# Kernel optimization log

Hardware: AMD Instinct MI355X
Metric: run time of the kernel (lower is better)

## Reference

```python
import jax, jax.numpy as jnp
import numpy as np

B, L, C, H, K = 2, 2048, 1024, 16, 32
Dh = C // H


def setup_inputs() -> dict:
    key = jax.random.key(0)
    ks = jax.random.split(key, 6)
    x = jax.random.normal(ks[0], (B, L, C), dtype=jnp.float32)
    # indices: self index first, then K-1 random neighbors (shared across batch & heads)
    self_idx = jnp.arange(L, dtype=jnp.int32).reshape(1, L, 1)
    rand_idx = jax.random.randint(ks[1], (1, L, K - 1), 0, L, dtype=jnp.int32)
    idx = jnp.concatenate([self_idx, rand_idx], axis=-1)  # (1, L, K)
    s = 1.0 / np.sqrt(C)
    Wq = jax.random.normal(ks[2], (C, C), dtype=jnp.float32) * s
    Wk = jax.random.normal(ks[3], (C, C), dtype=jnp.float32) * s
    Wv = jax.random.normal(ks[4], (C, C), dtype=jnp.float32) * s
    Wo = jax.random.normal(ks[5], (C, C), dtype=jnp.float32) * s
    return {"x": x, "idx": idx, "Wq": Wq, "Wk": Wk, "Wv": Wv, "Wo": Wo}


def reference(x, idx, Wq, Wk, Wv, Wo):
    # projections (torch Linear: y = x @ W.T), reshape to (B, H, L, Dh)
    def heads(y):
        return y.reshape(B, L, H, Dh).transpose(0, 2, 1, 3)

    q = heads(x @ Wq.T)
    k = heads(x @ Wk.T)
    v = heads(x @ Wv.T)

    idx0 = idx[0]  # (L, K) shared across batch and heads
    k_n = jnp.take(k, idx0, axis=2)  # (B, H, L, K, Dh)
    v_n = jnp.take(v, idx0, axis=2)  # (B, H, L, K, Dh)

    q = q / jnp.sqrt(jnp.asarray(Dh, q.dtype))
    attn = jnp.einsum("bhld,bhlkd->bhlk", q, k_n)
    attn = jax.nn.softmax(attn, axis=-1)
    out = jnp.einsum("bhlk,bhlkd->bhld", attn, v_n)
    out = out.transpose(0, 2, 1, 3).reshape(B, L, C)
    return out @ Wo.T
```

## Files before the change

### kernel.cpp

```cpp
#include <hip/hip_runtime.h>
#include <hip/hip_bf16.h>

#define B_  2
#define L_  2048
#define C_  1024
#define H_  16
#define K_  32
#define DH_ 64
#define M_  (B_ * L_)

typedef __hip_bfloat16 bf16;
typedef __attribute__((ext_vector_type(4))) float f32x4;
typedef __attribute__((ext_vector_type(8))) short short8;
typedef __attribute__((ext_vector_type(8))) unsigned short u16x8;

__device__ inline unsigned short f2bf(float f) {
    __hip_bfloat16 h = __float2bfloat16(f);
    return *reinterpret_cast<unsigned short*>(&h);
}
__device__ inline float bf2f(unsigned short u) {
    return __uint_as_float(((unsigned)u) << 16);
}
__device__ inline void gld_lds16(const bf16* g, bf16* l) {
    __builtin_amdgcn_global_load_lds(
        (const __attribute__((address_space(1))) void*)g,
        (__attribute__((address_space(3))) void*)l,
        16, 0, 0);
}

__global__ void __launch_bounds__(256) cvt_all(
    const float* __restrict__ x,  const float* __restrict__ wq,
    const float* __restrict__ wk, const float* __restrict__ wv,
    const float* __restrict__ wo,
    bf16* __restrict__ xb,  bf16* __restrict__ wqb, bf16* __restrict__ wkb,
    bf16* __restrict__ wvb, bf16* __restrict__ wob)
{
    int g = blockIdx.x * 256 + threadIdx.x;
    const float* src; bf16* dst; int o;
    if (g < 1048576)      { src = x;  dst = xb;  o = g; }
    else if (g < 1310720) { src = wq; dst = wqb; o = g - 1048576; }
    else if (g < 1572864) { src = wk; dst = wkb; o = g - 1310720; }
    else if (g < 1835008) { src = wv; dst = wvb; o = g - 1572864; }
    else                  { src = wo; dst = wob; o = g - 1835008; }
    float4 f = reinterpret_cast<const float4*>(src)[o];
    ushort4 u;
    u.x = f2bf(f.x); u.y = f2bf(f.y); u.z = f2bf(f.z); u.w = f2bf(f.w);
    reinterpret_cast<ushort4*>(dst)[o] = u;
}

struct GemmArgs {
    const bf16* A;
    const bf16* W[3];
    bf16* Yb[3];
    float* Yf;
    float scale0;
};

template<int OUT_F32>
__global__ void __launch_bounds__(256) gemm_nt(GemmArgs ga)
{
    __shared__ bf16 As[128 * 64];
    __shared__ bf16 Bs[128 * 64];

    const int m0  = blockIdx.x * 128;
    const int nt  = blockIdx.y;
    const int seg = nt >> 3;
    const int n0  = (nt & 7) * 128;
    const bf16* __restrict__ A = ga.A;
    const bf16* __restrict__ W = ga.W[seg];
    const float scale = (seg == 0) ? ga.scale0 : 1.0f;

    const int t    = threadIdx.x;
    const int lane = t & 63;
    const int w    = t >> 6;
    const int wm   = w >> 1;
    const int wn   = w & 1;

    const int subrow = lane >> 3;
    const int kc     = lane & 7;

    f32x4 acc[4][4] = {};

    for (int kt = 0; kt < 16; ++kt) {
        const int k0 = kt * 64;
        if (kt) __syncthreads();
        #pragma unroll
        for (int i = 0; i < 4; ++i) {
            const int r0  = w * 32 + i * 8;
            const int row = r0 + subrow;
            const int kcs = kc ^ (subrow & 7);
            gld_lds16(A + (size_t)(m0 + row) * 1024 + k0 + kcs * 8, As + r0 * 64);
        }
        #pragma unroll
        for (int i = 0; i < 4; ++i) {
            const int r0  = w * 32 + i * 8;
            const int row = r0 + subrow;
            const int kcs = kc ^ (subrow & 7);
            gld_lds16(W + (size_t)(n0 + row) * 1024 + k0 + kcs * 8, Bs + r0 * 64);
        }
        __syncthreads();
        #pragma unroll
        for (int ks = 0; ks < 2; ++ks) {
            short8 af[4], bfv[4];
            #pragma unroll
            for (int mf = 0; mf < 4; ++mf) {
                const int row    = wm * 64 + mf * 16 + (lane & 15);
                const int kchunk = ks * 4 + (lane >> 4);
                const int pc     = kchunk ^ (row & 7);
                af[mf] = *reinterpret_cast<const short8*>(As + row * 64 + pc * 8);
            }
            #pragma unroll
            for (int nf = 0; nf < 4; ++nf) {
                const int row    = wn * 64 + nf * 16 + (lane & 15);
                const int kchunk = ks * 4 + (lane >> 4);
                const int pc     = kchunk ^ (row & 7);
                bfv[nf] = *reinterpret_cast<const short8*>(Bs + row * 64 + pc * 8);
            }
            #pragma unroll
            for (int mf = 0; mf < 4; ++mf)
                #pragma unroll
                for (int nf = 0; nf < 4; ++nf)
                    acc[mf][nf] = __builtin_amdgcn_mfma_f32_16x16x32_bf16(
                        af[mf], bfv[nf], acc[mf][nf], 0, 0, 0);
        }
    }

    #pragma unroll
    for (int mf = 0; mf < 4; ++mf) {
        #pragma unroll
        for (int nf = 0; nf < 4; ++nf) {
            const int row = m0 + wm * 64 + mf * 16 + ((lane >> 4) << 2);
            const int col = n0 + wn * 64 + nf * 16 + (lane & 15);
            #pragma unroll
            for (int r = 0; r < 4; ++r) {
                const float val = acc[mf][nf][r] * scale;
                if constexpr (OUT_F32) {
                    ga.Yf[(size_t)(row + r) * 1024 + col] = val;
                } else {
                    ga.Yb[seg][(size_t)(row + r) * 1024 + col] = __float2bfloat16(val);
                }
            }
        }
    }
}

__global__ void __launch_bounds__(64) attn_knn(
    const bf16* __restrict__ qg, const bf16* __restrict__ kg,
    const bf16* __restrict__ vg, const int* __restrict__ idx,
    bf16* __restrict__ ao)
{
    const int wb = blockIdx.x;
    const int l  = blockIdx.y;
    const int b  = wb >> 2;
    const int wg = wb & 3;

    const int lane = threadIdx.x;
    const int hw   = lane >> 4;
    const int h    = wg * 4 + hw;
    const int sl   = lane & 15;
    const int half = sl >> 3;
    const int c8   = sl & 7;

    const size_t rowq = (size_t)b * L_ + l;
    const unsigned short* kg16 = reinterpret_cast<const unsigned short*>(kg);
    const unsigned short* vg16 = reinterpret_cast<const unsigned short*>(vg);

    int4 iv[4];
    #pragma unroll
    for (int i = 0; i < 4; ++i)
        iv[i] = reinterpret_cast<const int4*>(idx + l * K_ + half * 16)[i];

    u16x8 qv = *reinterpret_cast<const u16x8*>(
        reinterpret_cast<const unsigned short*>(qg) + rowq * C_ + h * DH_ + c8 * 8);
    float qf[8];
    #pragma unroll
    for (int e = 0; e < 8; ++e) qf[e] = bf2f(qv[e]);

    float s[16];
    #pragma unroll
    for (int jj = 0; jj < 16; ++jj) {
        const int4 q4 = iv[jj >> 2];
        const int row = (jj & 3) == 0 ? q4.x : (jj & 3) == 1 ? q4.y
                       : (jj & 3) == 2 ? q4.z : q4.w;
        const u16x8 kv = *reinterpret_cast<const u16x8*>(
            kg16 + ((size_t)b * L_ + row) * C_ + h * DH_ + c8 * 8);
        float acc = 0.f;
        #pragma unroll
        for (int e = 0; e < 8; ++e) acc += qf[e] * bf2f(kv[e]);
        s[jj] = acc;
    }

    #pragma unroll
    for (int jj = 0; jj < 16; ++jj) {
        float x = s[jj];
        x += __shfl_xor(x, 1, 16);
        x += __shfl_xor(x, 2, 16);
        x += __shfl_xor(x, 4, 16);
        s[jj] = x;
    }

    float m = s[0];
    #pragma unroll
    for (int jj = 1; jj < 16; ++jj) m = fmaxf(m, s[jj]);
    m = fmaxf(m, __shfl_xor(m, 8, 16));
    float ssum = 0.f;
    #pragma unroll
    for (int jj = 0; jj < 16; ++jj) { s[jj] = __expf(s[jj] - m); ssum += s[jj]; }
    ssum += __shfl_xor(ssum, 8, 16);
    const float inv = 1.0f / ssum;

    float acc[8] = {0.f, 0.f, 0.f, 0.f, 0.f, 0.f, 0.f, 0.f};
    #pragma unroll
    for (int jj = 0; jj < 16; ++jj) {
        const int4 q4 = iv[jj >> 2];
        const int row = (jj & 3) == 0 ? q4.x : (jj & 3) == 1 ? q4.y
                       : (jj & 3) == 2 ? q4.z : q4.w;
        const u16x8 vv = *reinterpret_cast<const u16x8*>(
            vg16 + ((size_t)b * L_ + row) * C_ + h * DH_ + c8 * 8);
        const float p = s[jj];
        #pragma unroll
        for (int e = 0; e < 8; ++e) acc[e] += p * bf2f(vv[e]);
    }
    #pragma unroll
    for (int e = 0; e < 8; ++e) acc[e] += __shfl_xor(acc[e], 8, 16);

    if (half == 0) {
        u16x8 o;
        #pragma unroll
        for (int e = 0; e < 8; ++e) o[e] = f2bf(acc[e] * inv);
        *reinterpret_cast<u16x8*>(ao + rowq * C_ + h * DH_ + c8 * 8) = o;
    }
}

extern "C" void kernel_launch(void* const* d_in, const int* in_sizes, int n_in,
                              void* d_out, int out_size, void* d_ws, size_t ws_size,
                              hipStream_t stream)
{
    const float* x  = (const float*)d_in[0];
    const int*   idx = (const int*)d_in[1];
    const float* Wq = (const float*)d_in[2];
    const float* Wk = (const float*)d_in[3];
    const float* Wv = (const float*)d_in[4];
    const float* Wo = (const float*)d_in[5];
    float* out = (float*)d_out;

    char* ws = (char*)d_ws;
    bf16* xb  = (bf16*)(ws + 0);
    bf16* wqb = (bf16*)(ws + 8388608);
    bf16* wkb = (bf16*)(ws + 10485760);
    bf16* wvb = (bf16*)(ws + 12582912);
    bf16* wob = (bf16*)(ws + 14680064);
    bf16* qb  = (bf16*)(ws + 16777216);
    bf16* kb  = (bf16*)(ws + 25165824);
    bf16* vb  = (bf16*)(ws + 33554432);
    bf16* ab  = (bf16*)(ws + 41943040);

    cvt_all<<<8192, 256, 0, stream>>>(x, Wq, Wk, Wv, Wo, xb, wqb, wkb, wvb, wob);

    GemmArgs g1;
    g1.A = xb;
    g1.W[0] = wqb; g1.W[1] = wkb; g1.W[2] = wvb;
    g1.Yb[0] = qb; g1.Yb[1] = kb; g1.Yb[2] = vb;
    g1.Yf = nullptr;
    g1.scale0 = 0.125f;
    gemm_nt<0><<<dim3(32, 24), 256, 0, stream>>>(g1);

    attn_knn<<<dim3(8, L_), 64, 0, stream>>>(qb, kb, vb, idx, ab);

    GemmArgs g2;
    g2.A = ab;
    g2.W[0] = wob; g2.W[1] = wob; g2.W[2] = wob;
    g2.Yb[0] = nullptr; g2.Yb[1] = nullptr; g2.Yb[2] = nullptr;
    g2.Yf = out;
    g2.scale0 = 1.0f;
    gemm_nt<1><<<dim3(32, 8), 256, 0, stream>>>(g2);
}
```

Baseline: 87.96 us.

## Add 256x256 double-buffered pipelined QKV GEMM with swizzled LDS

Replaces the QKV projection GEMM with a new kernel that uses 256x256 output tiles, 512 threads, and 128 KB of dynamic shared memory. The kernel double-buffers K-tiles, issuing global-to-LDS loads for the next tile while MFMAs run on the current one. It also XOR-swizzles LDS chunks to avoid bank conflicts and remaps block IDs for cache locality. The larger tiles cut operand reloads, but the grid shrinks to 192 blocks and the big LDS footprint limits occupancy. The output GEMM is simplified to an f32-only kernel.

After: 90.04 us. 1.02x slower.

```diff
diff --git a/kernel.cpp b/kernel.cpp
--- a/kernel.cpp
+++ b/kernel.cpp
@@ -48,27 +48,151 @@
     reinterpret_cast<ushort4*>(dst)[o] = u;
 }
 
+struct Gemm8Args {
+    const bf16* A;
+    const bf16* W[3];
+    bf16* Y[3];
+    float scale0;
+};
+
+#define SM_(buf, ab, kh, row, ch) sm[(buf)][(ab)][(kh)][(row)][(ch)]
+
+#define STAGE(bufn, ab, kh, rh, kt) {                                        \
+    const bf16* gb_ = ((ab) == 0)                                            \
+        ? A + (size_t)(m0 + (rh) * 128) * 1024                               \
+        : W + (size_t)(nw0 + (rh) * 128) * 1024;                             \
+    const bf16* src_ = gb_ + (size_t)srow * 1024 + (kt) * 64 + (kh) * 32     \
+                       + scc * 8;                                            \
+    bf16* lb_ = (bf16*)&SM_((bufn), (ab), (kh), (rh) * 128, 0)               \
+                + (size_t)(tid & ~63) * 8;                                   \
+    gld_lds16(src_, lb_);                                                    \
+}
+
+#define RD_A(cur, qm, kh) {                                                  \
+    _Pragma("unroll")                                                        \
+    for (int mf = 0; mf < 4; ++mf) {                                         \
+        const int R_  = wm * 128 + (qm) * 64 + mf * 16 + (lane & 15);        \
+        const int ch_ = (lane >> 4) ^ ((R_ >> 1) & 3);                       \
+        ak[mf] = SM_((cur), 0, (kh), R_, ch_);                               \
+    }                                                                        \
+}
+
+#define RD_B(cur, kh) {                                                      \
+    _Pragma("unroll")                                                        \
+    for (int nf = 0; nf < 4; ++nf) {                                         \
+        const int R_  = wn * 64 + nf * 16 + (lane & 15);                     \
+        const int ch_ = (lane >> 4) ^ ((R_ >> 1) & 3);                       \
+        bk[nf] = SM_((cur), 1, (kh), R_, ch_);                               \
+    }                                                                        \
+}
+
+#define MAC16(qm) {                                                          \
+    __builtin_amdgcn_s_setprio(1);                                           \
+    _Pragma("unroll")                                                        \
+    for (int mf = 0; mf < 4; ++mf)                                           \
+        _Pragma("unroll")                                                    \
+        for (int nf = 0; nf < 4; ++nf)                                       \
+            acc[(qm) * 4 + mf][nf] = __builtin_amdgcn_mfma_f32_16x16x32_bf16(\
+                ak[mf], bk[nf], acc[(qm) * 4 + mf][nf], 0, 0, 0);            \
+    __builtin_amdgcn_s_setprio(0);                                           \
+}
+
+#define KTILE_BODY(t, cur, nxt) {                                            \
+    const bool more_ = (t) + 1 < 16;                                         \
+                                                       \
+    asm volatile("s_waitcnt vmcnt(4)" ::: "memory");                         \
+    __builtin_amdgcn_s_barrier();                                            \
+    if (more_) { STAGE((nxt), 0, 0, 0, (t)+1); STAGE((nxt), 0, 0, 1, (t)+1);}\
+    RD_A((cur), 0, 0); RD_B((cur), 0);                                       \
+    MAC16(0);                                                                \
+                                                       \
+    if (more_) { STAGE((nxt), 1, 0, 0, (t)+1); STAGE((nxt), 1, 0, 1, (t)+1);}\
+    RD_A((cur), 1, 0);                                                       \
+    MAC16(1);                                                                \
+                                                       \
+    if (more_) asm volatile("s_waitcnt vmcnt(4)" ::: "memory");              \
+    else       asm volatile("s_waitcnt vmcnt(0)" ::: "memory");              \
+    __builtin_amdgcn_s_barrier();                                            \
+    if (more_) { STAGE((nxt), 0, 1, 0, (t)+1); STAGE((nxt), 0, 1, 1, (t)+1);}\
+    RD_A((cur), 0, 1); RD_B((cur), 1);                                       \
+    MAC16(0);                                                                \
+                                                       \
+    if (more_) { STAGE((nxt), 1, 1, 0, (t)+1); STAGE((nxt), 1, 1, 1, (t)+1);}\
+    RD_A((cur), 1, 1);                                                       \
+    MAC16(1);                                                                \
+}
+
+__global__ void __launch_bounds__(512, 2) gemm8_qkv(Gemm8Args ga)
+{
+    extern __shared__ __align__(16) char smraw[];
+    typedef short8 (*SmT)[2][2][256][4];
+    SmT sm = (SmT)smraw;
+
+    const int bid0 = blockIdx.x;
+    const int nid  = (bid0 & 7) * 24 + (bid0 >> 3);
+    const int bm   = nid & 15;
+    const int bn   = nid >> 4;
+    const int m0   = bm * 256;
+    const int seg  = bn >> 2;
+    const int nw0  = (bn & 3) * 256;
+
+    const bf16* __restrict__ A = ga.A;
+    const bf16* __restrict__ W = ga.W[seg];
+    bf16* __restrict__ Y = ga.Y[seg];
+    const float scale = (seg == 0) ? ga.scale0 : 1.0f;
+
+    const int tid  = threadIdx.x;
+    const int lane = tid & 63;
+    const int w    = tid >> 6;
+    const int wm   = w >> 2;
+    const int wn   = w & 3;
+
+    const int srow = tid >> 2;
+    const int scc  = (tid & 3) ^ ((srow >> 1) & 3);
+
+    f32x4 acc[8][4] = {};
+    short8 ak[4], bk[4];
+
+    STAGE(0, 0, 0, 0, 0); STAGE(0, 0, 0, 1, 0);
+    STAGE(0, 1, 0, 0, 0); STAGE(0, 1, 0, 1, 0);
+    STAGE(0, 0, 1, 0, 0); STAGE(0, 0, 1, 1, 0);
+    STAGE(0, 1, 1, 0, 0); STAGE(0, 1, 1, 1, 0);
+
+    #pragma unroll 1
+    for (int t = 0; t < 16; t += 2) {
+        KTILE_BODY(t,     0, 1);
+        KTILE_BODY(t + 1, 1, 0);
+    }
+
+    #pragma unroll
+    for (int am = 0; am < 8; ++am) {
+        #pragma unroll
+        for (int nf = 0; nf < 4; ++nf) {
+            const int row = m0 + wm * 128 + am * 16 + ((lane >> 4) << 2);
+            const int col = nw0 + wn * 64 + nf * 16 + (lane & 15);
+            #pragma unroll
+            for (int r = 0; r < 4; ++r)
+                Y[(size_t)(row + r) * 1024 + col] =
+                    __float2bfloat16(acc[am][nf][r] * scale);
+        }
+    }
+}
+
 struct GemmArgs {
     const bf16* A;
-    const bf16* W[3];
-    bf16* Yb[3];
+    const bf16* W;
     float* Yf;
-    float scale0;
 };
 
-template<int OUT_F32>
-__global__ void __launch_bounds__(256) gemm_nt(GemmArgs ga)
+__global__ void __launch_bounds__(256) gemm_nt_f32(GemmArgs ga)
 {
     __shared__ bf16 As[128 * 64];
     __shared__ bf16 Bs[128 * 64];
 
-    const int m0  = blockIdx.x * 128;
-    const int nt  = blockIdx.y;
-    const int seg = nt >> 3;
-    const int n0  = (nt & 7) * 128;
+    const int m0 = blockIdx.x * 128;
+    const int n0 = blockIdx.y * 128;
     const bf16* __restrict__ A = ga.A;
-    const bf16* __restrict__ W = ga.W[seg];
-    const float scale = (seg == 0) ? ga.scale0 : 1.0f;
+    const bf16* __restrict__ W = ga.W;
 
     const int t    = threadIdx.x;
     const int lane = t & 63;
@@ -132,14 +256,8 @@
             const int row = m0 + wm * 64 + mf * 16 + ((lane >> 4) << 2);
             const int col = n0 + wn * 64 + nf * 16 + (lane & 15);
             #pragma unroll
-            for (int r = 0; r < 4; ++r) {
-                const float val = acc[mf][nf][r] * scale;
-                if constexpr (OUT_F32) {
-                    ga.Yf[(size_t)(row + r) * 1024 + col] = val;
-                } else {
-                    ga.Yb[seg][(size_t)(row + r) * 1024 + col] = __float2bfloat16(val);
-                }
-            }
+            for (int r = 0; r < 4; ++r)
+                ga.Yf[(size_t)(row + r) * 1024 + col] = acc[mf][nf][r];
         }
     }
 }
@@ -164,6 +282,7 @@
     const size_t rowq = (size_t)b * L_ + l;
     const unsigned short* kg16 = reinterpret_cast<const unsigned short*>(kg);
     const unsigned short* vg16 = reinterpret_cast<const unsigned short*>(vg);
+    const size_t hoff = (size_t)h * DH_ + c8 * 8;
 
     int4 iv[4];
     #pragma unroll
@@ -171,7 +290,7 @@
         iv[i] = reinterpret_cast<const int4*>(idx + l * K_ + half * 16)[i];
 
     u16x8 qv = *reinterpret_cast<const u16x8*>(
-        reinterpret_cast<const unsigned short*>(qg) + rowq * C_ + h * DH_ + c8 * 8);
+        reinterpret_cast<const unsigned short*>(qg) + rowq * C_ + hoff);
     float qf[8];
     #pragma unroll
     for (int e = 0; e < 8; ++e) qf[e] = bf2f(qv[e]);
@@ -183,7 +302,7 @@
         const int row = (jj & 3) == 0 ? q4.x : (jj & 3) == 1 ? q4.y
                        : (jj & 3) == 2 ? q4.z : q4.w;
         const u16x8 kv = *reinterpret_cast<const u16x8*>(
-            kg16 + ((size_t)b * L_ + row) * C_ + h * DH_ + c8 * 8);
+            kg16 + ((size_t)b * L_ + row) * C_ + hoff);
         float acc = 0.f;
         #pragma unroll
         for (int e = 0; e < 8; ++e) acc += qf[e] * bf2f(kv[e]);
@@ -216,7 +335,7 @@
         const int row = (jj & 3) == 0 ? q4.x : (jj & 3) == 1 ? q4.y
                        : (jj & 3) == 2 ? q4.z : q4.w;
         const u16x8 vv = *reinterpret_cast<const u16x8*>(
-            vg16 + ((size_t)b * L_ + row) * C_ + h * DH_ + c8 * 8);
+            vg16 + ((size_t)b * L_ + row) * C_ + hoff);
         const float p = s[jj];
         #pragma unroll
         for (int e = 0; e < 8; ++e) acc[e] += p * bf2f(vv[e]);
@@ -228,7 +347,7 @@
         u16x8 o;
         #pragma unroll
         for (int e = 0; e < 8; ++e) o[e] = f2bf(acc[e] * inv);
-        *reinterpret_cast<u16x8*>(ao + rowq * C_ + h * DH_ + c8 * 8) = o;
+        *reinterpret_cast<u16x8*>(ao + rowq * C_ + hoff) = o;
     }
 }
 
@@ -257,21 +376,18 @@
 
     cvt_all<<<8192, 256, 0, stream>>>(x, Wq, Wk, Wv, Wo, xb, wqb, wkb, wvb, wob);
 
-    GemmArgs g1;
+    Gemm8Args g1;
     g1.A = xb;
     g1.W[0] = wqb; g1.W[1] = wkb; g1.W[2] = wvb;
-    g1.Yb[0] = qb; g1.Yb[1] = kb; g1.Yb[2] = vb;
-    g1.Yf = nullptr;
+    g1.Y[0] = qb;  g1.Y[1] = kb;  g1.Y[2] = vb;
     g1.scale0 = 0.125f;
-    gemm_nt<0><<<dim3(32, 24), 256, 0, stream>>>(g1);
+    gemm8_qkv<<<192, 512, 131072, stream>>>(g1);
 
     attn_knn<<<dim3(8, L_), 64, 0, stream>>>(qb, kb, vb, idx, ab);
 
     GemmArgs g2;
     g2.A = ab;
-    g2.W[0] = wob; g2.W[1] = wob; g2.W[2] = wob;
-    g2.Yb[0] = nullptr; g2.Yb[1] = nullptr; g2.Yb[2] = nullptr;
+    g2.W = wob;
     g2.Yf = out;
-    g2.scale0 = 1.0f;
-    gemm_nt<1><<<dim3(32, 8), 256, 0, stream>>>(g2);
-}
+    gemm_nt_f32<<<dim3(32, 8), 256, 0, stream>>>(g2);
+}
```

## Split kNN attention into separate QK-softmax and PV kernels via probability buffer

Applied to the files above, without the earlier changes.

Splits the fused kNN attention kernel into two launches. The first computes scores and softmax and writes normalized fp32 probabilities to a workspace buffer. The second reads them back and gathers V rows. The grid is also flattened to 1D with batch and head-group as the fastest index, so neighbouring blocks share the same query row. The likely aim is to cut register pressure and keep the K and V gathers in separate phases for better cache locality, at the cost of an extra launch and a round trip of the probability buffer.

Result: slower. 97.39 us (+10.7%).

```diff
diff --git a/kernel.cpp b/kernel.cpp
--- a/kernel.cpp
+++ b/kernel.cpp
@@ -144,15 +144,15 @@
     }
 }
 
-__global__ void __launch_bounds__(64) attn_knn(
+__global__ void __launch_bounds__(64) qk_knn(
     const bf16* __restrict__ qg, const bf16* __restrict__ kg,
-    const bf16* __restrict__ vg, const int* __restrict__ idx,
-    bf16* __restrict__ ao)
-{
-    const int wb = blockIdx.x;
-    const int l  = blockIdx.y;
-    const int b  = wb >> 2;
-    const int wg = wb & 3;
+    const int* __restrict__ idx, float* __restrict__ pg)
+{
+    const int bid  = blockIdx.x;
+    const int slot = bid & 7;
+    const int l    = bid >> 3;
+    const int b    = slot >> 2;
+    const int wg   = slot & 3;
 
     const int lane = threadIdx.x;
     const int hw   = lane >> 4;
@@ -163,7 +163,7 @@
 
     const size_t rowq = (size_t)b * L_ + l;
     const unsigned short* kg16 = reinterpret_cast<const unsigned short*>(kg);
-    const unsigned short* vg16 = reinterpret_cast<const unsigned short*>(vg);
+    const size_t hoff = (size_t)h * DH_ + c8 * 8;
 
     int4 iv[4];
     #pragma unroll
@@ -171,7 +171,7 @@
         iv[i] = reinterpret_cast<const int4*>(idx + l * K_ + half * 16)[i];
 
     u16x8 qv = *reinterpret_cast<const u16x8*>(
-        reinterpret_cast<const unsigned short*>(qg) + rowq * C_ + h * DH_ + c8 * 8);
+        reinterpret_cast<const unsigned short*>(qg) + rowq * C_ + hoff);
     float qf[8];
     #pragma unroll
     for (int e = 0; e < 8; ++e) qf[e] = bf2f(qv[e]);
@@ -183,7 +183,7 @@
         const int row = (jj & 3) == 0 ? q4.x : (jj & 3) == 1 ? q4.y
                        : (jj & 3) == 2 ? q4.z : q4.w;
         const u16x8 kv = *reinterpret_cast<const u16x8*>(
-            kg16 + ((size_t)b * L_ + row) * C_ + h * DH_ + c8 * 8);
+            kg16 + ((size_t)b * L_ + row) * C_ + hoff);
         float acc = 0.f;
         #pragma unroll
         for (int e = 0; e < 8; ++e) acc += qf[e] * bf2f(kv[e]);
@@ -209,15 +209,54 @@
     ssum += __shfl_xor(ssum, 8, 16);
     const float inv = 1.0f / ssum;
 
+    float2 w2;
+    w2.x = s[2 * c8]     * inv;
+    w2.y = s[2 * c8 + 1] * inv;
+    reinterpret_cast<float2*>(pg + (rowq * H_ + h) * K_ + half * 16)[c8] = w2;
+}
+
+__global__ void __launch_bounds__(64) pv_knn(
+    const float* __restrict__ pg, const bf16* __restrict__ vg,
+    const int* __restrict__ idx, bf16* __restrict__ ao)
+{
+    const int bid  = blockIdx.x;
+    const int slot = bid & 7;
+    const int l    = bid >> 3;
+    const int b    = slot >> 2;
+    const int wg   = slot & 3;
+
+    const int lane = threadIdx.x;
+    const int hw   = lane >> 4;
+    const int h    = wg * 4 + hw;
+    const int sl   = lane & 15;
+    const int half = sl >> 3;
+    const int c8   = sl & 7;
+
+    const size_t rowq = (size_t)b * L_ + l;
+    const unsigned short* vg16 = reinterpret_cast<const unsigned short*>(vg);
+    const size_t hoff = (size_t)h * DH_ + c8 * 8;
+
+    int4 iv[4];
+    #pragma unroll
+    for (int i = 0; i < 4; ++i)
+        iv[i] = reinterpret_cast<const int4*>(idx + l * K_ + half * 16)[i];
+
+    const float* pp = pg + (rowq * H_ + h) * K_ + half * 16;
+    float4 p4[4];
+    #pragma unroll
+    for (int i = 0; i < 4; ++i) p4[i] = reinterpret_cast<const float4*>(pp)[i];
+
     float acc[8] = {0.f, 0.f, 0.f, 0.f, 0.f, 0.f, 0.f, 0.f};
     #pragma unroll
     for (int jj = 0; jj < 16; ++jj) {
         const int4 q4 = iv[jj >> 2];
         const int row = (jj & 3) == 0 ? q4.x : (jj & 3) == 1 ? q4.y
                        : (jj & 3) == 2 ? q4.z : q4.w;
+        const float4 pq = p4[jj >> 2];
+        const float p = (jj & 3) == 0 ? pq.x : (jj & 3) == 1 ? pq.y
+                       : (jj & 3) == 2 ? pq.z : pq.w;
         const u16x8 vv = *reinterpret_cast<const u16x8*>(
-            vg16 + ((size_t)b * L_ + row) * C_ + h * DH_ + c8 * 8);
-        const float p = s[jj];
+            vg16 + ((size_t)b * L_ + row) * C_ + hoff);
         #pragma unroll
         for (int e = 0; e < 8; ++e) acc[e] += p * bf2f(vv[e]);
     }
@@ -227,8 +266,8 @@
     if (half == 0) {
         u16x8 o;
         #pragma unroll
-        for (int e = 0; e < 8; ++e) o[e] = f2bf(acc[e] * inv);
-        *reinterpret_cast<u16x8*>(ao + rowq * C_ + h * DH_ + c8 * 8) = o;
+        for (int e = 0; e < 8; ++e) o[e] = f2bf(acc[e]);
+        *reinterpret_cast<u16x8*>(ao + rowq * C_ + hoff) = o;
     }
 }
 
@@ -254,6 +293,7 @@
     bf16* kb  = (bf16*)(ws + 25165824);
     bf16* vb  = (bf16*)(ws + 33554432);
     bf16* ab  = (bf16*)(ws + 41943040);
+    float* pb = (float*)(ws + 50331648);
 
     cvt_all<<<8192, 256, 0, stream>>>(x, Wq, Wk, Wv, Wo, xb, wqb, wkb, wvb, wob);
 
@@ -265,7 +305,8 @@
     g1.scale0 = 0.125f;
     gemm_nt<0><<<dim3(32, 24), 256, 0, stream>>>(g1);
 
-    attn_knn<<<dim3(8, L_), 64, 0, stream>>>(qb, kb, vb, idx, ab);
+    qk_knn<<<L_ * 8, 64, 0, stream>>>(qb, kb, idx, pb);
+    pv_knn<<<L_ * 8, 64, 0, stream>>>(pb, vb, idx, ab);
 
     GemmArgs g2;
     g2.A = ab;
```
